# Kernel tuning notes

Measured on AMD Instinct MI355X. Metric: run time of the kernel, lower is better.

## Reference

```python
import jax, jax.numpy as jnp
import numpy as np

B, S, H, L = 8, 4096, 768, 256   # batch, seq_len, hidden_size, num_lines (= line_ids.max()+1)
ATT_HID = 1024                    # attention MLP hidden dim from nn.Linear(hidden,1024)


def setup_inputs() -> dict:
    key = jax.random.key(0)
    k0, k1, k2, k3 = jax.random.split(key, 4)
    token_hidden = jax.random.normal(k0, (B, S, H), dtype=jnp.float32)
    line_ids = jax.random.randint(k1, (B, S), 0, L)  # all valid; -1 would mark invalid
    W1 = jax.random.normal(k2, (H, ATT_HID), dtype=jnp.float32) * 0.02
    b1 = jnp.zeros((ATT_HID,), jnp.float32)
    W2 = jax.random.normal(k3, (ATT_HID, 1), dtype=jnp.float32) * 0.02
    b2 = jnp.zeros((1,), jnp.float32)
    return {"token_hidden": token_hidden, "line_ids": line_ids,
            "W1": W1, "b1": b1, "W2": W2, "b2": b2}


def reference(token_hidden, line_ids, W1, b1, W2, b2):
    b, s, h = token_hidden.shape
    num_lines = L
    n_seg = b * num_lines + 1  # last segment is a dump slot for invalid (-1) tokens

    # attention scores: Linear -> tanh -> Linear, squeeze(-1)  [b, s]
    scores = (jnp.tanh(token_hidden @ W1 + b1) @ W2 + b2)[..., 0]

    valid = (line_ids >= 0).reshape(-1)                                   # [b*s]
    seg = jnp.where(line_ids >= 0,
                    jnp.arange(b)[:, None] * num_lines + line_ids,
                    b * num_lines).reshape(-1)                            # [b*s]
    s_flat = jnp.where(valid, scores.reshape(-1), -jnp.inf)

    # segment-wise stable softmax
    m = jax.ops.segment_max(s_flat, seg, num_segments=n_seg)
    m = jnp.where(jnp.isfinite(m), m, 0.0)  # empty segments -> safe 0
    e = jnp.where(valid, jnp.exp(scores.reshape(-1) - m[seg]), 0.0)
    denom = jax.ops.segment_sum(e, seg, num_segments=n_seg)
    w = e / jnp.maximum(denom[seg], 1e-20)                                # [b*s]

    # weighted sum of tokens per (batch, line) segment
    feats = jax.ops.segment_sum(token_hidden.reshape(-1, h) * w[:, None],
                                seg, num_segments=n_seg)
    line_features = feats[: b * num_lines].reshape(b, num_lines, h)

    counts = jax.ops.segment_sum(valid.astype(jnp.float32), seg, num_segments=n_seg)
    line_mask = counts[: b * num_lines].reshape(b, num_lines) > 0
    return line_features, line_mask
```

## Files before the change

### kernel.cpp

```cpp
#include <hip/hip_runtime.h>
#include <hip/hip_bf16.h>
#include <string.h>

#define M_TOK 32768
#define H_DIM 768
#define AH    1024
#define NSEG  2048
#define CAP   96

typedef __attribute__((ext_vector_type(8))) __bf16 bf16x8;
typedef __attribute__((ext_vector_type(4))) float f32x4;

__device__ __forceinline__ float tanh_fast(float x) {
  float e = __expf(2.0f * x);
  return 1.0f - 2.0f * __builtin_amdgcn_rcpf(e + 1.0f);
}

__global__ __launch_bounds__(256) void convert_x(
    const float4* __restrict__ in, uint2* __restrict__ out) {
  int i = blockIdx.x * 256 + threadIdx.x;
  float4 v = in[i];
  __hip_bfloat16 h[4] = {__float2bfloat16(v.x), __float2bfloat16(v.y),
                         __float2bfloat16(v.z), __float2bfloat16(v.w)};
  uint2 p;
  memcpy(&p, h, 8);
  out[i] = p;
}

__global__ __launch_bounds__(256) void transpose_w1(
    const float* __restrict__ W1, __hip_bfloat16* __restrict__ W1t) {
  __shared__ float tile[32][33];
  int nt = blockIdx.x & 31, ktile = blockIdx.x >> 5;
  int n0 = nt * 32, k0 = ktile * 32;
  int tx = threadIdx.x & 31, ty = threadIdx.x >> 5;
  for (int r = ty; r < 32; r += 8)
    tile[r][tx] = W1[(size_t)(k0 + r) * AH + n0 + tx];
  __syncthreads();
  for (int r = ty; r < 32; r += 8)
    W1t[(size_t)(n0 + r) * H_DIM + k0 + tx] = __float2bfloat16(tile[tx][r]);
}

template <bool USE_XB>
__global__ __launch_bounds__(256) void attn_score_kernel(
    const __hip_bfloat16* __restrict__ Xbg, const float* __restrict__ Xf,
    const __hip_bfloat16* __restrict__ W1tg, const float* __restrict__ b1g,
    const float* __restrict__ W2g, float* __restrict__ scores) {
  __shared__ __align__(16) __bf16 As[128 * 32];
  __shared__ __align__(16) __bf16 Bs[128 * 32];

  const int tid = threadIdx.x;
  const int bid = blockIdx.x;
  const int xcd = bid & 7;
  const int s   = bid >> 3;
  const int m0  = (xcd * 32 + (s >> 3)) * 128;
  const int n0  = (s & 7) * 128;
  const int lane = tid & 63;
  const int wave = tid >> 6;
  const int wm   = (wave >> 1) * 64;
  const int wn   = (wave & 1) * 64;
  const int q8   = (lane >> 4) * 8;
  const int ml   = lane & 15;

  const __bf16* Xb = (const __bf16*)Xbg;
  const __bf16* W  = (const __bf16*)W1tg;

  const int rowoff = tid >> 2;
  const int colk   = (tid & 3) * 8;

  f32x4 acc[4][4];
#pragma unroll
  for (int i = 0; i < 4; i++)
#pragma unroll
    for (int j = 0; j < 4; j++) acc[i][j] = (f32x4)0.f;

  for (int kt = 0; kt < H_DIM; kt += 32) {
#pragma unroll
    for (int r = 0; r < 2; ++r) {
      if (USE_XB) {
        const __bf16* ga = Xb + (size_t)(m0 + r * 64 + rowoff) * H_DIM + kt + colk;
        __builtin_amdgcn_global_load_lds(
            (const __attribute__((address_space(1))) void*)ga,
            (__attribute__((address_space(3))) void*)&As[(r * 256 + tid) * 8],
            16, 0, 0);
      } else {
        const float* ga = Xf + (size_t)(m0 + r * 64 + rowoff) * H_DIM + kt + colk;
        float4 v0 = *(const float4*)ga;
        float4 v1 = *(const float4*)(ga + 4);
        __hip_bfloat16 h[8] = {
            __float2bfloat16(v0.x), __float2bfloat16(v0.y),
            __float2bfloat16(v0.z), __float2bfloat16(v0.w),
            __float2bfloat16(v1.x), __float2bfloat16(v1.y),
            __float2bfloat16(v1.z), __float2bfloat16(v1.w)};
        memcpy(&As[(r * 256 + tid) * 8], h, 16);
      }
      const __bf16* gb = W + (size_t)(n0 + r * 64 + rowoff) * H_DIM + kt + colk;
      __builtin_amdgcn_global_load_lds(
          (const __attribute__((address_space(1))) void*)gb,
          (__attribute__((address_space(3))) void*)&Bs[(r * 256 + tid) * 8],
          16, 0, 0);
    }
    __syncthreads();

    bf16x8 af[4], bf[4];
#pragma unroll
    for (int i = 0; i < 4; i++)
      af[i] = *(const bf16x8*)&As[(wm + i * 16 + ml) * 32 + q8];
#pragma unroll
    for (int j = 0; j < 4; j++)
      bf[j] = *(const bf16x8*)&Bs[(wn + j * 16 + ml) * 32 + q8];

#pragma unroll
    for (int i = 0; i < 4; i++)
#pragma unroll
      for (int j = 0; j < 4; j++)
        acc[i][j] = __builtin_amdgcn_mfma_f32_16x16x32_bf16(af[i], bf[j],
                                                            acc[i][j], 0, 0, 0);
    __syncthreads();
  }

  float b1v[4], w2v[4];
#pragma unroll
  for (int j = 0; j < 4; j++) {
    int n = n0 + wn + j * 16 + ml;
    b1v[j] = b1g[n];
    w2v[j] = W2g[n];
  }
  const int q4 = (lane >> 4) * 4;
#pragma unroll
  for (int i = 0; i < 4; i++) {
#pragma unroll
    for (int p = 0; p < 4; p++) {
      float t = 0.f;
#pragma unroll
      for (int j = 0; j < 4; j++)
        t += tanh_fast(acc[i][j][p] + b1v[j]) * w2v[j];
      t += __shfl_xor(t, 1);
      t += __shfl_xor(t, 2);
      t += __shfl_xor(t, 4);
      t += __shfl_xor(t, 8);
      if (ml == 0) atomicAdd(&scores[m0 + wm + i * 16 + q4 + p], t);
    }
  }
}

__global__ __launch_bounds__(256) void scatter_bucket(
    const int* __restrict__ line_ids, int* __restrict__ cursor,
    int* __restrict__ order) {
  int t = blockIdx.x * 256 + threadIdx.x;
  int lid = line_ids[t];
  if (lid >= 0) {
    int seg = (t >> 12) * 256 + lid;
    int pos = atomicAdd(&cursor[seg], 1);
    if (pos < CAP) order[seg * CAP + pos] = t;
  }
}

__global__ __launch_bounds__(256) void aggregate_kernel(
    const float4* __restrict__ X4, const float* __restrict__ scores,
    const int* __restrict__ cursor, const int* __restrict__ order,
    float4* __restrict__ out4, float* __restrict__ out_mask) {
  __shared__ float sw[CAP];
  __shared__ int   sidx[CAP];
  __shared__ float wred[4];
  const int seg = blockIdx.x;
  const int tid = threadIdx.x;
  int cnt = cursor[seg];
  if (cnt > CAP) cnt = CAP;
  if (tid == 0) out_mask[seg] = cnt > 0 ? 1.f : 0.f;
  if (cnt == 0) {
    if (tid < H_DIM / 4) out4[(size_t)seg * (H_DIM / 4) + tid] =
        make_float4(0.f, 0.f, 0.f, 0.f);
    return;
  }
  const int lane = tid & 63, wave = tid >> 6;
  float lmax = -3.4e38f;
  if (tid < cnt) {
    int idx = order[seg * CAP + tid];
    sidx[tid] = idx;
    float sc = scores[idx];
    sw[tid] = sc;
    lmax = sc;
  }
#pragma unroll
  for (int d = 1; d < 64; d <<= 1) lmax = fmaxf(lmax, __shfl_xor(lmax, d));
  if (lane == 0) wred[wave] = lmax;
  __syncthreads();
  float m = fmaxf(fmaxf(wred[0], wred[1]), fmaxf(wred[2], wred[3]));
  float lsum = 0.f;
  if (tid < cnt) {
    float e = __expf(sw[tid] - m);
    sw[tid] = e;
    lsum = e;
  }
#pragma unroll
  for (int d = 1; d < 64; d <<= 1) lsum += __shfl_xor(lsum, d);
  __syncthreads();
  if (lane == 0) wred[wave] = lsum;
  __syncthreads();
  float denom = wred[0] + wred[1] + wred[2] + wred[3];
  float inv = __builtin_amdgcn_rcpf(fmaxf(denom, 1e-20f));
  if (tid < cnt) sw[tid] *= inv;
  __syncthreads();
  if (tid < H_DIM / 4) {
    float4 acc = make_float4(0.f, 0.f, 0.f, 0.f);
    for (int t = 0; t < cnt; ++t) {
      float w = sw[t];
      float4 v = X4[(size_t)sidx[t] * (H_DIM / 4) + tid];
      acc.x += w * v.x; acc.y += w * v.y; acc.z += w * v.z; acc.w += w * v.w;
    }
    out4[(size_t)seg * (H_DIM / 4) + tid] = acc;
  }
}

extern "C" void kernel_launch(void* const* d_in, const int* in_sizes, int n_in,
                              void* d_out, int out_size, void* d_ws, size_t ws_size,
                              hipStream_t stream) {
  const float* X        = (const float*)d_in[0];
  const int*   line_ids = (const int*)d_in[1];
  const float* W1       = (const float*)d_in[2];
  const float* b1       = (const float*)d_in[3];
  const float* W2       = (const float*)d_in[4];

  const size_t XB_BYTES   = (size_t)M_TOK * H_DIM * 2;
  const size_t REST_BYTES = 1572864 + 131072 + 8192 + (size_t)NSEG * CAP * 4;
  bool useXb = ws_size >= XB_BYTES + REST_BYTES;

  char* p = (char*)d_ws;
  __hip_bfloat16* Xb = useXb ? (__hip_bfloat16*)p : nullptr;
  if (useXb) p += XB_BYTES;
  __hip_bfloat16* W1t = (__hip_bfloat16*)p;  p += 1572864;
  float* scores  = (float*)p;                p += 131072;
  int*   cursor  = (int*)p;                  p += 8192;
  int*   order   = (int*)p;                  p += (size_t)NSEG * CAP * 4;

  float* out_feats = (float*)d_out;
  float* out_mask  = out_feats + (size_t)NSEG * H_DIM;

  hipMemsetAsync(scores, 0, 131072 + 8192, stream);

  if (useXb)
    convert_x<<<(M_TOK * H_DIM) / 4 / 256, 256, 0, stream>>>(
        (const float4*)X, (uint2*)Xb);
  transpose_w1<<<768, 256, 0, stream>>>(W1, W1t);
  if (useXb)
    attn_score_kernel<true><<<2048, 256, 0, stream>>>(Xb, X, W1t, b1, W2, scores);
  else
    attn_score_kernel<false><<<2048, 256, 0, stream>>>(nullptr, X, W1t, b1, W2, scores);
  scatter_bucket<<<M_TOK / 256, 256, 0, stream>>>(line_ids, cursor, order);
  aggregate_kernel<<<NSEG, 256, 0, stream>>>((const float4*)X, scores, cursor,
                                             order, (float4*)out_feats, out_mask);
}
```

Baseline: 264.3 us.

## Drop separate bf16 conversion pass, merge prep kernels, unroll aggregate gather

Removes the standalone X fp32->bf16 conversion kernel and always converts X in-register inside the GEMM tile load, eliminating a full write and re-read of a bf16 copy of X. Merges the W1 transpose and line bucketing into one launch to cut launch overhead, and unrolls the aggregate gather loop by four for more memory-level parallelism. In exchange, the GEMM A-tile loads now go through registers rather than direct global-to-LDS copies, which may lengthen the main loop and reduce overlap.

Measured after the change: 271.4 us. +2.7%, slower.

```diff
diff --git a/kernel.cpp b/kernel.cpp
--- a/kernel.cpp
+++ b/kernel.cpp
@@ -16,35 +16,35 @@
   return 1.0f - 2.0f * __builtin_amdgcn_rcpf(e + 1.0f);
 }
 
-__global__ __launch_bounds__(256) void convert_x(
-    const float4* __restrict__ in, uint2* __restrict__ out) {
-  int i = blockIdx.x * 256 + threadIdx.x;
-  float4 v = in[i];
-  __hip_bfloat16 h[4] = {__float2bfloat16(v.x), __float2bfloat16(v.y),
-                         __float2bfloat16(v.z), __float2bfloat16(v.w)};
-  uint2 p;
-  memcpy(&p, h, 8);
-  out[i] = p;
-}
-
-__global__ __launch_bounds__(256) void transpose_w1(
-    const float* __restrict__ W1, __hip_bfloat16* __restrict__ W1t) {
+__global__ __launch_bounds__(256) void prep_kernel(
+    const float* __restrict__ W1, __hip_bfloat16* __restrict__ W1t,
+    const int* __restrict__ line_ids, int* __restrict__ cursor,
+    int* __restrict__ order) {
   __shared__ float tile[32][33];
-  int nt = blockIdx.x & 31, ktile = blockIdx.x >> 5;
-  int n0 = nt * 32, k0 = ktile * 32;
-  int tx = threadIdx.x & 31, ty = threadIdx.x >> 5;
-  for (int r = ty; r < 32; r += 8)
-    tile[r][tx] = W1[(size_t)(k0 + r) * AH + n0 + tx];
-  __syncthreads();
-  for (int r = ty; r < 32; r += 8)
-    W1t[(size_t)(n0 + r) * H_DIM + k0 + tx] = __float2bfloat16(tile[tx][r]);
-}
-
-template <bool USE_XB>
+  if (blockIdx.x < 768) {
+    int nt = blockIdx.x & 31, ktile = blockIdx.x >> 5;
+    int n0 = nt * 32, k0 = ktile * 32;
+    int tx = threadIdx.x & 31, ty = threadIdx.x >> 5;
+    for (int r = ty; r < 32; r += 8)
+      tile[r][tx] = W1[(size_t)(k0 + r) * AH + n0 + tx];
+    __syncthreads();
+    for (int r = ty; r < 32; r += 8)
+      W1t[(size_t)(n0 + r) * H_DIM + k0 + tx] = __float2bfloat16(tile[tx][r]);
+  } else {
+    int t = (blockIdx.x - 768) * 256 + threadIdx.x;
+    int lid = line_ids[t];
+    if (lid >= 0) {
+      int seg = (t >> 12) * 256 + lid;
+      int pos = atomicAdd(&cursor[seg], 1);
+      if (pos < CAP) order[seg * CAP + pos] = t;
+    }
+  }
+}
+
 __global__ __launch_bounds__(256) void attn_score_kernel(
-    const __hip_bfloat16* __restrict__ Xbg, const float* __restrict__ Xf,
-    const __hip_bfloat16* __restrict__ W1tg, const float* __restrict__ b1g,
-    const float* __restrict__ W2g, float* __restrict__ scores) {
+    const float* __restrict__ Xf, const __hip_bfloat16* __restrict__ W1tg,
+    const float* __restrict__ b1g, const float* __restrict__ W2g,
+    float* __restrict__ scores) {
   __shared__ __align__(16) __bf16 As[128 * 32];
   __shared__ __align__(16) __bf16 Bs[128 * 32];
 
@@ -61,8 +61,7 @@
   const int q8   = (lane >> 4) * 8;
   const int ml   = lane & 15;
 
-  const __bf16* Xb = (const __bf16*)Xbg;
-  const __bf16* W  = (const __bf16*)W1tg;
+  const __bf16* W = (const __bf16*)W1tg;
 
   const int rowoff = tid >> 2;
   const int colk   = (tid & 3) * 8;
@@ -76,28 +75,20 @@
   for (int kt = 0; kt < H_DIM; kt += 32) {
 #pragma unroll
     for (int r = 0; r < 2; ++r) {
-      if (USE_XB) {
-        const __bf16* ga = Xb + (size_t)(m0 + r * 64 + rowoff) * H_DIM + kt + colk;
-        __builtin_amdgcn_global_load_lds(
-            (const __attribute__((address_space(1))) void*)ga,
-            (__attribute__((address_space(3))) void*)&As[(r * 256 + tid) * 8],
-            16, 0, 0);
-      } else {
-        const float* ga = Xf + (size_t)(m0 + r * 64 + rowoff) * H_DIM + kt + colk;
-        float4 v0 = *(const float4*)ga;
-        float4 v1 = *(const float4*)(ga + 4);
-        __hip_bfloat16 h[8] = {
-            __float2bfloat16(v0.x), __float2bfloat16(v0.y),
-            __float2bfloat16(v0.z), __float2bfloat16(v0.w),
-            __float2bfloat16(v1.x), __float2bfloat16(v1.y),
-            __float2bfloat16(v1.z), __float2bfloat16(v1.w)};
-        memcpy(&As[(r * 256 + tid) * 8], h, 16);
-      }
       const __bf16* gb = W + (size_t)(n0 + r * 64 + rowoff) * H_DIM + kt + colk;
       __builtin_amdgcn_global_load_lds(
           (const __attribute__((address_space(1))) void*)gb,
           (__attribute__((address_space(3))) void*)&Bs[(r * 256 + tid) * 8],
           16, 0, 0);
+      const float* ga = Xf + (size_t)(m0 + r * 64 + rowoff) * H_DIM + kt + colk;
+      float4 v0 = *(const float4*)ga;
+      float4 v1 = *(const float4*)(ga + 4);
+      __hip_bfloat16 h[8] = {
+          __float2bfloat16(v0.x), __float2bfloat16(v0.y),
+          __float2bfloat16(v0.z), __float2bfloat16(v0.w),
+          __float2bfloat16(v1.x), __float2bfloat16(v1.y),
+          __float2bfloat16(v1.z), __float2bfloat16(v1.w)};
+      memcpy(&As[(r * 256 + tid) * 8], h, 16);
     }
     __syncthreads();
 
@@ -140,18 +131,6 @@
       t += __shfl_xor(t, 8);
       if (ml == 0) atomicAdd(&scores[m0 + wm + i * 16 + q4 + p], t);
     }
-  }
-}
-
-__global__ __launch_bounds__(256) void scatter_bucket(
-    const int* __restrict__ line_ids, int* __restrict__ cursor,
-    int* __restrict__ order) {
-  int t = blockIdx.x * 256 + threadIdx.x;
-  int lid = line_ids[t];
-  if (lid >= 0) {
-    int seg = (t >> 12) * 256 + lid;
-    int pos = atomicAdd(&cursor[seg], 1);
-    if (pos < CAP) order[seg * CAP + pos] = t;
   }
 }
 
@@ -168,8 +147,8 @@
   if (cnt > CAP) cnt = CAP;
   if (tid == 0) out_mask[seg] = cnt > 0 ? 1.f : 0.f;
   if (cnt == 0) {
-    if (tid < H_DIM / 4) out4[(size_t)seg * (H_DIM / 4) + tid] =
-        make_float4(0.f, 0.f, 0.f, 0.f);
+    if (tid < H_DIM / 4)
+      out4[(size_t)seg * (H_DIM / 4) + tid] = make_float4(0.f, 0.f, 0.f, 0.f);
     return;
   }
   const int lane = tid & 63, wave = tid >> 6;
@@ -202,10 +181,24 @@
   if (tid < cnt) sw[tid] *= inv;
   __syncthreads();
   if (tid < H_DIM / 4) {
+    const float4* base = X4 + tid;
     float4 acc = make_float4(0.f, 0.f, 0.f, 0.f);
-    for (int t = 0; t < cnt; ++t) {
+    int t = 0;
+    for (; t + 4 <= cnt; t += 4) {
+      int i0 = sidx[t], i1 = sidx[t + 1], i2 = sidx[t + 2], i3 = sidx[t + 3];
+      float4 v0 = base[(size_t)i0 * (H_DIM / 4)];
+      float4 v1 = base[(size_t)i1 * (H_DIM / 4)];
+      float4 v2 = base[(size_t)i2 * (H_DIM / 4)];
+      float4 v3 = base[(size_t)i3 * (H_DIM / 4)];
+      float w0 = sw[t], w1 = sw[t + 1], w2 = sw[t + 2], w3 = sw[t + 3];
+      acc.x += w0 * v0.x + w1 * v1.x + w2 * v2.x + w3 * v3.x;
+      acc.y += w0 * v0.y + w1 * v1.y + w2 * v2.y + w3 * v3.y;
+      acc.z += w0 * v0.z + w1 * v1.z + w2 * v2.z + w3 * v3.z;
+      acc.w += w0 * v0.w + w1 * v1.w + w2 * v2.w + w3 * v3.w;
+    }
+    for (; t < cnt; ++t) {
       float w = sw[t];
-      float4 v = X4[(size_t)sidx[t] * (H_DIM / 4) + tid];
+      float4 v = base[(size_t)sidx[t] * (H_DIM / 4)];
       acc.x += w * v.x; acc.y += w * v.y; acc.z += w * v.z; acc.w += w * v.w;
     }
     out4[(size_t)seg * (H_DIM / 4) + tid] = acc;
@@ -221,13 +214,7 @@
   const float* b1       = (const float*)d_in[3];
   const float* W2       = (const float*)d_in[4];
 
-  const size_t XB_BYTES   = (size_t)M_TOK * H_DIM * 2;
-  const size_t REST_BYTES = 1572864 + 131072 + 8192 + (size_t)NSEG * CAP * 4;
-  bool useXb = ws_size >= XB_BYTES + REST_BYTES;
-
   char* p = (char*)d_ws;
-  __hip_bfloat16* Xb = useXb ? (__hip_bfloat16*)p : nullptr;
-  if (useXb) p += XB_BYTES;
   __hip_bfloat16* W1t = (__hip_bfloat16*)p;  p += 1572864;
   float* scores  = (float*)p;                p += 131072;
   int*   cursor  = (int*)p;                  p += 8192;
@@ -238,15 +225,9 @@
 
   hipMemsetAsync(scores, 0, 131072 + 8192, stream);
 
-  if (useXb)
-    convert_x<<<(M_TOK * H_DIM) / 4 / 256, 256, 0, stream>>>(
-        (const float4*)X, (uint2*)Xb);
-  transpose_w1<<<768, 256, 0, stream>>>(W1, W1t);
-  if (useXb)
-    attn_score_kernel<true><<<2048, 256, 0, stream>>>(Xb, X, W1t, b1, W2, scores);
-  else
-    attn_score_kernel<false><<<2048, 256, 0, stream>>>(nullptr, X, W1t, b1, W2, scores);
-  scatter_bucket<<<M_TOK / 256, 256, 0, stream>>>(line_ids, cursor, order);
+  prep_kernel<<<768 + M_TOK / 256, 256, 0, stream>>>(W1, W1t, line_ids,
+                                                     cursor, order);
+  attn_score_kernel<<<2048, 256, 0, stream>>>(X, W1t, b1, W2, scores);
   aggregate_kernel<<<NSEG, 256, 0, stream>>>((const float4*)X, scores, cursor,
                                              order, (float4*)out_feats, out_mask);
 }
```
